# Optimization experiments

Hardware: AMD Instinct MI355X
Metric: run time of the kernel (lower is better)

The kernel has to match this reference:

```python
import jax, jax.numpy as jnp
import numpy as np

N, E, G = 100000, 1600000, 512
F_IN, H = 226, 128
BN_EPS = 1e-5

def _params(key):
    ks = jax.random.split(key, 34)
    p = {}
    dims = [(F_IN, H), (H, H), (H, H), (H, H)]
    i = 0
    for l, (din, dout) in enumerate(dims, start=1):
        p[f"W{l}a"] = jax.random.normal(ks[i], (din, dout), jnp.float32) * 0.05; i += 1
        p[f"b{l}a"] = jnp.zeros((dout,), jnp.float32)
        p[f"g{l}"] = jnp.ones((dout,), jnp.float32)
        p[f"be{l}"] = jnp.zeros((dout,), jnp.float32)
        p[f"rm{l}"] = jax.random.normal(ks[i], (dout,), jnp.float32) * 0.01; i += 1
        p[f"rv{l}"] = jnp.ones((dout,), jnp.float32)
        p[f"W{l}b"] = jax.random.normal(ks[i], (dout, dout), jnp.float32) * 0.05; i += 1
        p[f"b{l}b"] = jnp.zeros((dout,), jnp.float32)
    p["Wl"] = jax.random.normal(ks[i], (H, 1), jnp.float32) * 0.05
    p["bl"] = jnp.zeros((1,), jnp.float32)
    return p

def setup_inputs() -> dict:
    key = jax.random.key(0)
    k1, k2, k3, kp = jax.random.split(key, 4)
    inp = {
        "x": jax.random.normal(k1, (N, F_IN), jnp.float32),
        "edge_index": jax.random.randint(k2, (2, E), 0, N, jnp.int64),
        "batch": jnp.sort(jax.random.randint(k3, (N,), 0, G, jnp.int64)),
    }
    inp.update(_params(kp))
    return inp

def _gin_layer(x, src, dst, Wa, ba, g, be, rm, rv, Wb, bb):
    # GINConv (eps=0): mlp(x + sum_{j in N(i)} x_j)
    agg = jax.ops.segment_sum(x[src], dst, num_segments=N)  # [N,H] scatter-add
    h = (x + agg) @ Wa + ba
    h = g * (h - rm) * jax.lax.rsqrt(rv + BN_EPS) + be  # eval-mode BatchNorm1d
    h = jax.nn.relu(h)
    h = h @ Wb + bb
    return jax.nn.relu(h)  # outer F.relu after conv

def reference(x, edge_index, batch,
              W1a, b1a, g1, be1, rm1, rv1, W1b, b1b,
              W2a, b2a, g2, be2, rm2, rv2, W2b, b2b,
              W3a, b3a, g3, be3, rm3, rv3, W3b, b3b,
              W4a, b4a, g4, be4, rm4, rv4, W4b, b4b,
              Wl, bl):
    src, dst = edge_index[0], edge_index[1]
    h = _gin_layer(x, src, dst, W1a, b1a, g1, be1, rm1, rv1, W1b, b1b)
    h = _gin_layer(h, src, dst, W2a, b2a, g2, be2, rm2, rv2, W2b, b2b)
    h = _gin_layer(h, src, dst, W3a, b3a, g3, be3, rm3, rv3, W3b, b3b)
    h = _gin_layer(h, src, dst, W4a, b4a, g4, be4, rm4, rv4, W4b, b4b)
    # global mean pool over graphs
    sums = jax.ops.segment_sum(h, batch, num_segments=G)          # [G,H]
    cnts = jax.ops.segment_sum(jnp.ones((N,), h.dtype), batch, num_segments=G)
    pooled = sums / jnp.maximum(cnts, 1.0)[:, None]
    return pooled @ Wl + bl  # [G,1]
```

## Files before the change

kernel.cpp:

```cpp
#include <hip/hip_runtime.h>

#define NN 100000
#define NE 1600000
#define NG 512
#define FIN 226
#define HD 128
#define BN_EPS 1e-5f
#define NBUK 196
#define BCAP 10016

typedef __attribute__((ext_vector_type(8))) __bf16 bf16x8;
typedef __attribute__((ext_vector_type(8))) short short8;
typedef __attribute__((ext_vector_type(8))) unsigned short ushort8;
typedef __attribute__((ext_vector_type(4))) float f32x4;
typedef __attribute__((ext_vector_type(2))) float f32x2;

#define BC(x) __builtin_bit_cast(bf16x8, x)

__device__ inline unsigned short f2bf(float v) {
  unsigned u = __builtin_bit_cast(unsigned, v);
  return (unsigned short)((u + 0x7FFFu + ((u >> 16) & 1u)) >> 16);
}
__device__ inline float bf2f(unsigned short b) {
  return __builtin_bit_cast(float, (unsigned)b << 16);
}

__global__ __launch_bounds__(256) void k_bucket(const int* __restrict__ src,
                                                const int* __restrict__ dst,
                                                int* __restrict__ gcur,
                                                unsigned* __restrict__ pairs) {
  __shared__ int sd[4096];
  __shared__ int ss[4096];
  __shared__ int sh[NBUK];
  __shared__ int sexcl[NBUK];
  __shared__ int scur[NBUK];
  __shared__ int sbase[NBUK];
  __shared__ int wsum[4];
  const int tid = threadIdx.x;
  const int i0 = blockIdx.x * 4096;
  #pragma unroll
  for (int j = 0; j < 16; ++j) {
    int e = i0 + j * 256 + tid;
    sd[j * 256 + tid] = (e < NE) ? __builtin_nontemporal_load(dst + e) : -1;
    ss[j * 256 + tid] = (e < NE) ? __builtin_nontemporal_load(src + e) : 0;
  }
  if (tid < NBUK) sh[tid] = 0;
  __syncthreads();
  #pragma unroll
  for (int j = 0; j < 16; ++j) {
    int d = sd[j * 256 + tid];
    if (d >= 0) atomicAdd(&sh[d >> 9], 1);
  }
  __syncthreads();
  {
    int v = (tid < NBUK) ? sh[tid] : 0;
    int lane = tid & 63, w = tid >> 6;
    int incl = v;
    #pragma unroll
    for (int o = 1; o < 64; o <<= 1) {
      int u = __shfl_up(incl, o);
      if (lane >= o) incl += u;
    }
    if (lane == 63) wsum[w] = incl;
    __syncthreads();
    int off = 0;
    for (int k = 0; k < w; ++k) off += wsum[k];
    if (tid < NBUK) {
      int ex = off + incl - v;
      sexcl[tid] = ex;
      scur[tid] = ex;
      sbase[tid] = (v > 0) ? atomicAdd(&gcur[tid], v) : 0;
    }
  }
  __syncthreads();
  #pragma unroll
  for (int j = 0; j < 16; ++j) {
    int d = sd[j * 256 + tid];
    if (d >= 0) {
      int b = d >> 9;
      int lp = atomicAdd(&scur[b], 1);
      unsigned pk = ((unsigned)(d & 511) << 17) | (unsigned)ss[j * 256 + tid];
      pairs[(size_t)b * BCAP + sbase[b] + (lp - sexcl[b])] = pk;
    }
  }
}

__global__ __launch_bounds__(256) void k_bscan(const int* __restrict__ gcur,
                                               int* __restrict__ bucket_base,
                                               int* __restrict__ row_ptr) {
  __shared__ int wsum[4];
  const int tid = threadIdx.x;
  int v = (tid < NBUK) ? gcur[tid] : 0;
  int lane = tid & 63, w = tid >> 6;
  int incl = v;
  #pragma unroll
  for (int o = 1; o < 64; o <<= 1) {
    int u = __shfl_up(incl, o);
    if (lane >= o) incl += u;
  }
  if (lane == 63) wsum[w] = incl;
  __syncthreads();
  int off = 0;
  for (int k = 0; k < w; ++k) off += wsum[k];
  if (tid < NBUK) bucket_base[tid] = off + incl - v;
  if (tid == 0) row_ptr[NN] = NE;
}

__global__ __launch_bounds__(256) void k_pass2(const unsigned* __restrict__ pairs,
                                               const int* __restrict__ gcur,
                                               const int* __restrict__ bucket_base,
                                               int* __restrict__ row_ptr,
                                               int* __restrict__ col_idx) {
  __shared__ unsigned spk[BCAP];
  __shared__ int h[512];
  __shared__ int cur[512];
  __shared__ int wsum[4];
  const int b = blockIdx.x;
  const int tid = threadIdx.x;
  const int cnt = gcur[b];
  const int base = bucket_base[b];
  for (int i = tid; i < cnt; i += 256) spk[i] = pairs[(size_t)b * BCAP + i];
  h[tid] = 0; h[tid + 256] = 0;
  __syncthreads();
  for (int i = tid; i < cnt; i += 256) atomicAdd(&h[spk[i] >> 17], 1);
  __syncthreads();
  int c0 = h[2 * tid], c1 = h[2 * tid + 1];
  {
    int v = c0 + c1;
    int lane = tid & 63, w = tid >> 6;
    int incl = v;
    #pragma unroll
    for (int o = 1; o < 64; o <<= 1) {
      int u = __shfl_up(incl, o);
      if (lane >= o) incl += u;
    }
    if (lane == 63) wsum[w] = incl;
    __syncthreads();
    int off = 0;
    for (int k = 0; k < w; ++k) off += wsum[k];
    int e0 = off + incl - v;
    int e1 = e0 + c0;
    int node0 = b * 512 + 2 * tid;
    if (node0 < NN) row_ptr[node0] = base + e0;
    if (node0 + 1 < NN) row_ptr[node0 + 1] = base + e1;
    cur[2 * tid] = e0;
    cur[2 * tid + 1] = e1;
  }
  __syncthreads();
  for (int i = tid; i < cnt; i += 256) {
    unsigned pk = spk[i];
    int dl = pk >> 17;
    int p = atomicAdd(&cur[dl], 1);
    col_idx[base + p] = (int)(pk & 0x1FFFFu);
  }
}

struct PrepArgs {
  const float* W[9];
  const float* g[9];
  const float* rv[9];
  unsigned short* out[9];
  int k0[9];
  int K[9];
  const float* ba[4];
  const float* gg[4];
  const float* be[4];
  const float* rm[4];
  const float* rvv[4];
  float* bout;
};

__global__ __launch_bounds__(256) void k_prep(PrepArgs a) {
  int id = blockIdx.x * 256 + threadIdx.x;
  if (id < 9 * 16384) {
    int chunk = id >> 14;
    int r = id & 16383;
    int kk = r >> 7;
    int n = r & 127;
    float s = a.g[chunk] ? a.g[chunk][n] * rsqrtf(a.rv[chunk][n] + BN_EPS) : 1.f;
    int kg = a.k0[chunk] + kk;
    float v = (kg < a.K[chunk]) ? a.W[chunk][(size_t)kg * HD + n] * s : 0.f;
    unsigned short hb = f2bf(v);
    unsigned short lb = f2bf(v - bf2f(hb));
    int idx = n * 128 + (kk ^ ((n & 7) << 3));
    a.out[chunk][idx] = hb;
    a.out[chunk][16384 + idx] = lb;
  } else {
    int t = id - 9 * 16384;
    if (t < 512) {
      int l = t >> 7, c = t & 127;
      float s = a.gg[l][c] * rsqrtf(a.rvv[l][c] + BN_EPS);
      a.bout[l * 128 + c] = a.ba[l][c] * s + a.be[l][c] - a.rm[l][c] * s;
    }
  }
}

__global__ __launch_bounds__(256) void k_mgemm1(const float* __restrict__ A,
                                                const unsigned short* __restrict__ Wz,
                                                unsigned short* __restrict__ out,
                                                int K, int nchunks) {
  __shared__ unsigned short sW[32768];
  const int tid = threadIdx.x;
  const int wv = tid >> 6, ln = tid & 63;
  const int l15 = ln & 15, l4 = ln >> 4;
  const int m0 = blockIdx.x * 128 + wv * 32;
  f32x4 acc[2][8] = {};
  const int sw = (l15 & 7) << 3;
  int kofs[4];
  #pragma unroll
  for (int ks = 0; ks < 4; ++ks) kofs[ks] = (((ks * 32 + l4 * 8) ^ sw)) + l15 * 128;

  for (int c = 0; c < nchunks; ++c) {
    {
      const ushort8* src = (const ushort8*)(Wz + (size_t)c * 32768);
      ushort8* dst = (ushort8*)sW;
      #pragma unroll
      for (int i = 0; i < 16; ++i) dst[tid + i * 256] = src[tid + i * 256];
    }
    __syncthreads();
    const int kc = c * 128;
    #pragma unroll
    for (int ks = 0; ks < 4; ++ks) {
      const int kbase = kc + ks * 32 + l4 * 8;
      const bool tail = (kc + ks * 32 + 32) > K;
      short8 ah[2], al[2];
      #pragma unroll
      for (int mf = 0; mf < 2; ++mf) {
        const int row = m0 + mf * 16 + l15;
        float v[8];
        if (row < NN && !tail) {
          const f32x2* ap = (const f32x2*)(A + (size_t)row * K + kbase);
          #pragma unroll
          for (int q = 0; q < 4; ++q) {
            f32x2 t = __builtin_nontemporal_load(ap + q);
            v[2 * q] = t[0]; v[2 * q + 1] = t[1];
          }
        } else if (row < NN) {
          #pragma unroll
          for (int j = 0; j < 8; ++j) {
            int k = kbase + j;
            v[j] = (k < K) ? A[(size_t)row * K + k] : 0.f;
          }
        } else {
          #pragma unroll
          for (int j = 0; j < 8; ++j) v[j] = 0.f;
        }
        #pragma unroll
        for (int j = 0; j < 8; ++j) {
          unsigned short hb = f2bf(v[j]);
          ah[mf][j] = (short)hb;
          al[mf][j] = (short)f2bf(v[j] - bf2f(hb));
        }
      }
      #pragma unroll
      for (int n = 0; n < 8; ++n) {
        const int idx = n * 2048 + kofs[ks];
        short8 bh = *(const short8*)&sW[idx];
        short8 bl = *(const short8*)&sW[idx + 16384];
        #pragma unroll
        for (int mf = 0; mf < 2; ++mf) {
          acc[mf][n] = __builtin_amdgcn_mfma_f32_16x16x32_bf16(BC(ah[mf]), BC(bh), acc[mf][n], 0, 0, 0);
          acc[mf][n] = __builtin_amdgcn_mfma_f32_16x16x32_bf16(BC(ah[mf]), BC(bl), acc[mf][n], 0, 0, 0);
          acc[mf][n] = __builtin_amdgcn_mfma_f32_16x16x32_bf16(BC(al[mf]), BC(bh), acc[mf][n], 0, 0, 0);
        }
      }
    }
    __syncthreads();
  }
  #pragma unroll
  for (int mf = 0; mf < 2; ++mf) {
    #pragma unroll
    for (int n = 0; n < 8; ++n) {
      const int col = n * 16 + l15;
      #pragma unroll
      for (int r = 0; r < 4; ++r) {
        const int row = m0 + mf * 16 + l4 * 4 + r;
        if (row < NN) out[(size_t)row * HD + col] = f2bf(acc[mf][n][r]);
      }
    }
  }
}

template <int BIAS, int RELU>
__global__ __launch_bounds__(256) void k_mgemmB(const unsigned short* __restrict__ A,
                                                const unsigned short* __restrict__ Wz,
                                                const float* __restrict__ bias,
                                                unsigned short* __restrict__ out) {
  __shared__ unsigned short sW[32768];
  const int tid = threadIdx.x;
  const int wv = tid >> 6, ln = tid & 63;
  const int l15 = ln & 15, l4 = ln >> 4;
  const int m0 = blockIdx.x * 128 + wv * 32;
  f32x4 acc[2][8] = {};
  const int sw = (l15 & 7) << 3;
  {
    const ushort8* src = (const ushort8*)Wz;
    ushort8* dst = (ushort8*)sW;
    #pragma unroll
    for (int i = 0; i < 16; ++i) dst[tid + i * 256] = src[tid + i * 256];
  }
  __syncthreads();
  #pragma unroll
  for (int ks = 0; ks < 4; ++ks) {
    const int kbase = ks * 32 + l4 * 8;
    short8 a[2];
    #pragma unroll
    for (int mf = 0; mf < 2; ++mf) {
      const int row = m0 + mf * 16 + l15;
      if (row < NN) a[mf] = *(const short8*)(A + (size_t)row * HD + kbase);
      else a[mf] = short8{0, 0, 0, 0, 0, 0, 0, 0};
    }
    const int kof = (kbase ^ sw) + l15 * 128;
    #pragma unroll
    for (int n = 0; n < 8; ++n) {
      const int idx = n * 2048 + kof;
      short8 bh = *(const short8*)&sW[idx];
      short8 bl = *(const short8*)&sW[idx + 16384];
      #pragma unroll
      for (int mf = 0; mf < 2; ++mf) {
        acc[mf][n] = __builtin_amdgcn_mfma_f32_16x16x32_bf16(BC(a[mf]), BC(bh), acc[mf][n], 0, 0, 0);
        acc[mf][n] = __builtin_amdgcn_mfma_f32_16x16x32_bf16(BC(a[mf]), BC(bl), acc[mf][n], 0, 0, 0);
      }
    }
  }
  #pragma unroll
  for (int mf = 0; mf < 2; ++mf) {
    #pragma unroll
    for (int n = 0; n < 8; ++n) {
      const int col = n * 16 + l15;
      float bv = BIAS ? bias[col] : 0.f;
      #pragma unroll
      for (int r = 0; r < 4; ++r) {
        const int row = m0 + mf * 16 + l4 * 4 + r;
        if (row < NN) {
          float o = acc[mf][n][r] + bv;
          if (RELU) o = fmaxf(o, 0.f);
          out[(size_t)row * HD + col] = f2bf(o);
        }
      }
    }
  }
}

__global__ __launch_bounds__(256) void k_fused(const unsigned short* __restrict__ H,
                                               const unsigned short* __restrict__ Wzb,
                                               const float* __restrict__ bb,
                                               const unsigned short* __restrict__ Wza,
                                               unsigned short* __restrict__ Yout) {
  __shared__ unsigned short sB[16384];
  __shared__ unsigned short sA2[16384];
  __shared__ unsigned short sX[8192];
  const int tid = threadIdx.x;
  const int wv = tid >> 6, ln = tid & 63;
  const int l15 = ln & 15, l4 = ln >> 4;
  const int m0 = blockIdx.x * 128 + wv * 32;
  const int sw = (l15 & 7) << 3;
  f32x4 acc2[2][8] = {};

  short8 a[2][4];
  #pragma unroll
  for (int mf = 0; mf < 2; ++mf) {
    const int row = m0 + mf * 16 + l15;
    #pragma unroll
    for (int ks = 0; ks < 4; ++ks) {
      if (row < NN) a[mf][ks] = *(const short8*)(H + (size_t)row * HD + ks * 32 + l4 * 8);
      else a[mf][ks] = short8{0, 0, 0, 0, 0, 0, 0, 0};
    }
  }

  #pragma unroll 1
  for (int p = 0; p < 2; ++p) {
    {
      ushort8* d = (ushort8*)sB;
      const ushort8* s1 = (const ushort8*)(Wzb + p * 8192);
      const ushort8* s2 = (const ushort8*)(Wzb + 16384 + p * 8192);
      #pragma unroll
      for (int i = 0; i < 4; ++i) d[tid + i * 256] = s1[tid + i * 256];
      #pragma unroll
      for (int i = 0; i < 4; ++i) d[1024 + tid + i * 256] = s2[tid + i * 256];
    }
    {
      ushort8* d2 = (ushort8*)sA2;
      const ushort8* sa = (const ushort8*)Wza;
      #pragma unroll
      for (int i = 0; i < 4; ++i) {
        int idx = tid + i * 256;
        int n = idx >> 3, q8 = idx & 7;
        d2[idx] = sa[n * 16 + p * 8 + q8];
      }
      #pragma unroll
      for (int i = 0; i < 4; ++i) {
        int idx = tid + i * 256;
        int n = idx >> 3, q8 = idx & 7;
        d2[1024 + idx] = sa[2048 + n * 16 + p * 8 + q8];
      }
    }
    __syncthreads();

    f32x4 acc1[2][4] = {};
    #pragma unroll
    for (int ks = 0; ks < 4; ++ks) {
      const int kof = (ks * 32 + l4 * 8) ^ sw;
      #pragma unroll
      for (int nf = 0; nf < 4; ++nf) {
        const int idx = (nf * 16 + l15) * 128 + kof;
        short8 bh = *(const short8*)&sB[idx];
        short8 bl = *(const short8*)&sB[8192 + idx];
        #pragma unroll
        for (int mf = 0; mf < 2; ++mf) {
          acc1[mf][nf] = __builtin_amdgcn_mfma_f32_16x16x32_bf16(BC(a[mf][ks]), BC(bh), acc1[mf][nf], 0, 0, 0);
          acc1[mf][nf] = __builtin_amdgcn_mfma_f32_16x16x32_bf16(BC(a[mf][ks]), BC(bl), acc1[mf][nf], 0, 0, 0);
        }
      }
    }
    #pragma unroll
    for (int mf = 0; mf < 2; ++mf) {
      #pragma unroll
      for (int nf = 0; nf < 4; ++nf) {
        const int colL = nf * 16 + l15;
        const float bv = bb[p * 64 + colL];
        #pragma unroll
        for (int r = 0; r < 4; ++r) {
          const int rowL = wv * 32 + mf * 16 + l4 * 4 + r;
          sX[rowL * 64 + (colL ^ ((rowL & 7) << 3))] = f2bf(fmaxf(acc1[mf][nf][r] + bv, 0.f));
        }
      }
    }
    #pragma unroll
    for (int ks2 = 0; ks2 < 2; ++ks2) {
      const int xkof = (ks2 * 32 + l4 * 8) ^ sw;
      short8 xf[2];
      #pragma unroll
      for (int mf = 0; mf < 2; ++mf) {
        const int rowL = wv * 32 + mf * 16 + l15;
        xf[mf] = *(const short8*)&sX[rowL * 64 + xkof];
      }
      #pragma unroll
      for (int nf = 0; nf < 8; ++nf) {
        const int idx = (nf * 16 + l15) * 64 + xkof;
        short8 wh = *(const short8*)&sA2[idx];
        short8 wl = *(const short8*)&sA2[8192 + idx];
        #pragma unroll
        for (int mf = 0; mf < 2; ++mf) {
          acc2[mf][nf] = __builtin_amdgcn_mfma_f32_16x16x32_bf16(BC(xf[mf]), BC(wh), acc2[mf][nf], 0, 0, 0);
          acc2[mf][nf] = __builtin_amdgcn_mfma_f32_16x16x32_bf16(BC(xf[mf]), BC(wl), acc2[mf][nf], 0, 0, 0);
        }
      }
    }
    __syncthreads();
  }
  #pragma unroll
  for (int mf = 0; mf < 2; ++mf) {
    #pragma unroll
    for (int n = 0; n < 8; ++n) {
      const int col = n * 16 + l15;
      #pragma unroll
      for (int r = 0; r < 4; ++r) {
        const int row = m0 + mf * 16 + l4 * 4 + r;
        if (row < NN) Yout[(size_t)row * HD + col] = f2bf(acc2[mf][n][r]);
      }
    }
  }
}

__global__ __launch_bounds__(256) void k_agg(const unsigned short* __restrict__ y,
                                             const int* __restrict__ row_ptr,
                                             const int* __restrict__ col_idx,
                                             const float* __restrict__ bias,
                                             unsigned short* __restrict__ h) {
  const int node = blockIdx.x * 4 + (threadIdx.x >> 6);
  const int ln = threadIdx.x & 63;
  const int l15 = ln & 15, grp = ln >> 4;
  if (node >= NN) return;
  float acc[8] = {};
  const int beg = row_ptr[node], end = row_ptr[node + 1];
  int e = beg;
  for (; e + 16 <= end; e += 16) {
    const int s0 = __builtin_nontemporal_load(col_idx + e + grp);
    const int s1 = __builtin_nontemporal_load(col_idx + e + 4 + grp);
    const int s2 = __builtin_nontemporal_load(col_idx + e + 8 + grp);
    const int s3 = __builtin_nontemporal_load(col_idx + e + 12 + grp);
    const ushort8 v0 = *(const ushort8*)(y + (size_t)s0 * HD + l15 * 8);
    const ushort8 v1 = *(const ushort8*)(y + (size_t)s1 * HD + l15 * 8);
    const ushort8 v2 = *(const ushort8*)(y + (size_t)s2 * HD + l15 * 8);
    const ushort8 v3 = *(const ushort8*)(y + (size_t)s3 * HD + l15 * 8);
    #pragma unroll
    for (int j = 0; j < 8; ++j)
      acc[j] += (bf2f((unsigned short)v0[j]) + bf2f((unsigned short)v1[j])) +
                (bf2f((unsigned short)v2[j]) + bf2f((unsigned short)v3[j]));
  }
  for (; e + 8 <= end; e += 8) {
    const int s0 = __builtin_nontemporal_load(col_idx + e + grp);
    const int s1 = __builtin_nontemporal_load(col_idx + e + 4 + grp);
    const ushort8 v0 = *(const ushort8*)(y + (size_t)s0 * HD + l15 * 8);
    const ushort8 v1 = *(const ushort8*)(y + (size_t)s1 * HD + l15 * 8);
    #pragma unroll
    for (int j = 0; j < 8; ++j)
      acc[j] += bf2f((unsigned short)v0[j]) + bf2f((unsigned short)v1[j]);
  }
  if (e + 4 <= end) {
    const int s0 = __builtin_nontemporal_load(col_idx + e + grp);
    const ushort8 v0 = *(const ushort8*)(y + (size_t)s0 * HD + l15 * 8);
    #pragma unroll
    for (int j = 0; j < 8; ++j) acc[j] += bf2f((unsigned short)v0[j]);
    e += 4;
  }
  if (e + grp < end) {
    const int s0 = col_idx[e + grp];
    const ushort8 v0 = *(const ushort8*)(y + (size_t)s0 * HD + l15 * 8);
    #pragma unroll
    for (int j = 0; j < 8; ++j) acc[j] += bf2f((unsigned short)v0[j]);
  }
  #pragma unroll
  for (int j = 0; j < 8; ++j) {
    acc[j] += __shfl_xor(acc[j], 16);
    acc[j] += __shfl_xor(acc[j], 32);
  }
  const ushort8 sv = *(const ushort8*)(y + (size_t)node * HD + l15 * 8);
  const f32x4* b4 = (const f32x4*)(bias + l15 * 8);
  const f32x4 b0 = b4[0], b1 = b4[1];
  ushort8 o;
  #pragma unroll
  for (int j = 0; j < 8; ++j) {
    const float bj = (j < 4) ? b0[j] : b1[j - 4];
    o[j] = (unsigned short)f2bf(fmaxf(acc[j] + bf2f((unsigned short)sv[j]) + bj, 0.f));
  }
  if (grp == 0) *(ushort8*)(h + (size_t)node * HD + l15 * 8) = o;
}

__global__ __launch_bounds__(256) void k_pool2(const unsigned short* __restrict__ h,
                                               const int* __restrict__ batch,
                                               const float* __restrict__ Wl,
                                               float* __restrict__ sums,
                                               float* __restrict__ cnts) {
  __shared__ float sb[NG];
  __shared__ int sc[NG];
  const int tid = threadIdx.x;
  for (int i = tid; i < NG; i += 256) { sb[i] = 0.f; sc[i] = 0; }
  __syncthreads();
  const int wv = tid >> 6, ln = tid & 63;
  const float2 w2 = reinterpret_cast<const float2*>(Wl)[ln];
  #pragma unroll 1
  for (int i = 0; i < 16; ++i) {
    const int node = blockIdx.x * 64 + wv * 16 + i;
    if (node < NN) {
      const ushort2 hv = reinterpret_cast<const ushort2*>(h)[(size_t)node * 64 + ln];
      float d = bf2f(hv.x) * w2.x + bf2f(hv.y) * w2.y;
      #pragma unroll
      for (int off = 32; off > 0; off >>= 1) d += __shfl_down(d, off);
      if (ln == 0) {
        const int g = batch[node];
        atomicAdd(&sb[g], d);
        atomicAdd(&sc[g], 1);
      }
    }
  }
  __syncthreads();
  for (int i = tid; i < NG; i += 256)
    if (sc[i]) { atomicAdd(&sums[i], sb[i]); atomicAdd(&cnts[i], (float)sc[i]); }
}

__global__ void k_final(const float* __restrict__ sums, const float* __restrict__ cnts,
                        const float* __restrict__ bl, float* __restrict__ out) {
  int g = blockIdx.x * 256 + threadIdx.x;
  if (g < NG) out[g] = sums[g] / fmaxf(cnts[g], 1.f) + bl[0];
}

extern "C" void kernel_launch(void* const* d_in, const int* in_sizes, int n_in,
                              void* d_out, int out_size, void* d_ws, size_t ws_size,
                              hipStream_t stream) {
  const float* x = (const float*)d_in[0];
  const int* edges = (const int*)d_in[1];
  const int* batch = (const int*)d_in[2];
  const int* e_src = edges;
  const int* e_dst = edges + NE;
  const float* Wl = (const float*)d_in[35];
  const float* bl = (const float*)d_in[36];
  float* out = (float*)d_out;
  auto P = [&](int l, int which) -> const float* {
    return (const float*)d_in[3 + (l - 1) * 8 + which];
  };

  char* ws = (char*)d_ws;
  size_t off = 0;
  auto take = [&](size_t bytes) -> void* {
    void* p = ws + off;
    off = (off + bytes + 255) & ~(size_t)255;
    return p;
  };
  unsigned short* Y = (unsigned short*)take((size_t)NN * HD * 2);
  unsigned short* H = (unsigned short*)take((size_t)NN * HD * 2);
  unsigned short* X = (unsigned short*)take((size_t)NN * HD * 2);
  int* row_ptr = (int*)take((size_t)(NN + 1) * 4);
  int* col_idx = (int*)take((size_t)NE * 4);
  unsigned* pairs = (unsigned*)take((size_t)NBUK * BCAP * 4);
  int* gcur = (int*)take((size_t)NBUK * 4);
  int* bucket_base = (int*)take((size_t)NBUK * 4);
  unsigned short* Wza[4];
  unsigned short* Wzb[4];
  Wza[0] = (unsigned short*)take((size_t)2 * 32768 * 2);
  for (int l = 1; l < 4; ++l) Wza[l] = (unsigned short*)take((size_t)32768 * 2);
  for (int l = 0; l < 4; ++l) Wzb[l] = (unsigned short*)take((size_t)32768 * 2);
  float* bf = (float*)take((size_t)4 * HD * 4);
  float* psum = (float*)take((size_t)NG * 4 * 2);
  float* pcnt = psum + NG;

  hipMemsetAsync(gcur, 0, (size_t)NBUK * 4, stream);
  k_bucket<<<(NE + 4095) / 4096, 256, 0, stream>>>(e_src, e_dst, gcur, pairs);
  k_bscan<<<1, 256, 0, stream>>>(gcur, bucket_base, row_ptr);
  k_pass2<<<NBUK, 256, 0, stream>>>(pairs, gcur, bucket_base, row_ptr, col_idx);

  PrepArgs pa;
  for (int c = 0; c < 9; ++c) {
    if (c < 2) { pa.W[c] = P(1, 0); pa.g[c] = P(1, 2); pa.rv[c] = P(1, 5);
                 pa.out[c] = Wza[0] + c * 32768; pa.k0[c] = c * 128; pa.K[c] = FIN; }
    else if (c < 5) { int l = c - 1; pa.W[c] = P(l + 1, 0); pa.g[c] = P(l + 1, 2);
                      pa.rv[c] = P(l + 1, 5); pa.out[c] = Wza[l]; pa.k0[c] = 0; pa.K[c] = HD; }
    else { int l = c - 5; pa.W[c] = P(l + 1, 6); pa.g[c] = nullptr; pa.rv[c] = nullptr;
           pa.out[c] = Wzb[l]; pa.k0[c] = 0; pa.K[c] = HD; }
  }
  for (int l = 0; l < 4; ++l) {
    pa.ba[l] = P(l + 1, 1); pa.gg[l] = P(l + 1, 2); pa.be[l] = P(l + 1, 3);
    pa.rm[l] = P(l + 1, 4); pa.rvv[l] = P(l + 1, 5);
  }
  pa.bout = bf;
  k_prep<<<(9 * 16384 + 512 + 255) / 256, 256, 0, stream>>>(pa);

  hipMemsetAsync(psum, 0, (size_t)NG * 8, stream);

  const int gemm_grid = (NN + 127) / 128;
  k_mgemm1<<<gemm_grid, 256, 0, stream>>>(x, Wza[0], Y, FIN, 2);
  for (int l = 1; l <= 3; ++l) {
    k_agg<<<NN / 4, 256, 0, stream>>>(Y, row_ptr, col_idx, bf + (l - 1) * HD, H);
    k_fused<<<gemm_grid, 256, 0, stream>>>(H, Wzb[l - 1], P(l, 7), Wza[l], Y);
  }
  k_agg<<<NN / 4, 256, 0, stream>>>(Y, row_ptr, col_idx, bf + 3 * HD, H);
  k_mgemmB<1, 1><<<gemm_grid, 256, 0, stream>>>(H, Wzb[3], P(4, 7), X);
  k_pool2<<<(NN + 63) / 64, 256, 0, stream>>>(X, batch, Wl, psum, pcnt);
  k_final<<<(NG + 255) / 256, 256, 0, stream>>>(psum, pcnt, bl, out);
}
```

Measured before the change: 522.0 us.

## Drop split-bf16 weight low parts, fuse last GEMM into pooling, merge bucket scan

Weights are now stored as a single bf16 value instead of a hi/lo pair, which removes one MFMA per tile and halves the weight shared-memory loads and footprint. The final layer's second GEMM is fused with the mean-pool dot product, so the X intermediate is no longer written and read back. The bucket prefix scan is folded into k_pass2, which saves one kernel launch. The cost is lower numerical precision, since weight rounding error is no longer compensated.

```diff
diff --git a/kernel.cpp b/kernel.cpp
--- a/kernel.cpp
+++ b/kernel.cpp
@@ -85,40 +85,36 @@
   }
 }
 
-__global__ __launch_bounds__(256) void k_bscan(const int* __restrict__ gcur,
-                                               int* __restrict__ bucket_base,
-                                               int* __restrict__ row_ptr) {
-  __shared__ int wsum[4];
-  const int tid = threadIdx.x;
-  int v = (tid < NBUK) ? gcur[tid] : 0;
-  int lane = tid & 63, w = tid >> 6;
-  int incl = v;
-  #pragma unroll
-  for (int o = 1; o < 64; o <<= 1) {
-    int u = __shfl_up(incl, o);
-    if (lane >= o) incl += u;
-  }
-  if (lane == 63) wsum[w] = incl;
-  __syncthreads();
-  int off = 0;
-  for (int k = 0; k < w; ++k) off += wsum[k];
-  if (tid < NBUK) bucket_base[tid] = off + incl - v;
-  if (tid == 0) row_ptr[NN] = NE;
-}
-
 __global__ __launch_bounds__(256) void k_pass2(const unsigned* __restrict__ pairs,
                                                const int* __restrict__ gcur,
-                                               const int* __restrict__ bucket_base,
                                                int* __restrict__ row_ptr,
                                                int* __restrict__ col_idx) {
   __shared__ unsigned spk[BCAP];
   __shared__ int h[512];
   __shared__ int cur[512];
   __shared__ int wsum[4];
+  __shared__ int s_base;
   const int b = blockIdx.x;
   const int tid = threadIdx.x;
+  {
+    int v = (tid < NBUK) ? gcur[tid] : 0;
+    int lane = tid & 63, w = tid >> 6;
+    int incl = v;
+    #pragma unroll
+    for (int o = 1; o < 64; o <<= 1) {
+      int u = __shfl_up(incl, o);
+      if (lane >= o) incl += u;
+    }
+    if (lane == 63) wsum[w] = incl;
+    __syncthreads();
+    int off = 0;
+    for (int k = 0; k < w; ++k) off += wsum[k];
+    if (tid == b) s_base = off + incl - v;
+    if (b == 0 && tid == 0) row_ptr[NN] = NE;
+  }
   const int cnt = gcur[b];
-  const int base = bucket_base[b];
+  __syncthreads();
+  const int base = s_base;
   for (int i = tid; i < cnt; i += 256) spk[i] = pairs[(size_t)b * BCAP + i];
   h[tid] = 0; h[tid + 256] = 0;
   __syncthreads();
@@ -180,11 +176,8 @@
     float s = a.g[chunk] ? a.g[chunk][n] * rsqrtf(a.rv[chunk][n] + BN_EPS) : 1.f;
     int kg = a.k0[chunk] + kk;
     float v = (kg < a.K[chunk]) ? a.W[chunk][(size_t)kg * HD + n] * s : 0.f;
-    unsigned short hb = f2bf(v);
-    unsigned short lb = f2bf(v - bf2f(hb));
     int idx = n * 128 + (kk ^ ((n & 7) << 3));
-    a.out[chunk][idx] = hb;
-    a.out[chunk][16384 + idx] = lb;
+    a.out[chunk][idx] = f2bf(v);
   } else {
     int t = id - 9 * 16384;
     if (t < 512) {
@@ -199,7 +192,7 @@
                                                 const unsigned short* __restrict__ Wz,
                                                 unsigned short* __restrict__ out,
                                                 int K, int nchunks) {
-  __shared__ unsigned short sW[32768];
+  __shared__ unsigned short sW[16384];
   const int tid = threadIdx.x;
   const int wv = tid >> 6, ln = tid & 63;
   const int l15 = ln & 15, l4 = ln >> 4;
@@ -212,10 +205,10 @@
 
   for (int c = 0; c < nchunks; ++c) {
     {
-      const ushort8* src = (const ushort8*)(Wz + (size_t)c * 32768);
+      const ushort8* src = (const ushort8*)(Wz + (size_t)c * 16384);
       ushort8* dst = (ushort8*)sW;
       #pragma unroll
-      for (int i = 0; i < 16; ++i) dst[tid + i * 256] = src[tid + i * 256];
+      for (int i = 0; i < 8; ++i) dst[tid + i * 256] = src[tid + i * 256];
     }
     __syncthreads();
     const int kc = c * 128;
@@ -254,13 +247,10 @@
       }
       #pragma unroll
       for (int n = 0; n < 8; ++n) {
-        const int idx = n * 2048 + kofs[ks];
-        short8 bh = *(const short8*)&sW[idx];
-        short8 bl = *(const short8*)&sW[idx + 16384];
+        short8 bh = *(const short8*)&sW[n * 2048 + kofs[ks]];
         #pragma unroll
         for (int mf = 0; mf < 2; ++mf) {
           acc[mf][n] = __builtin_amdgcn_mfma_f32_16x16x32_bf16(BC(ah[mf]), BC(bh), acc[mf][n], 0, 0, 0);
-          acc[mf][n] = __builtin_amdgcn_mfma_f32_16x16x32_bf16(BC(ah[mf]), BC(bl), acc[mf][n], 0, 0, 0);
           acc[mf][n] = __builtin_amdgcn_mfma_f32_16x16x32_bf16(BC(al[mf]), BC(bh), acc[mf][n], 0, 0, 0);
         }
       }
@@ -276,67 +266,6 @@
       for (int r = 0; r < 4; ++r) {
         const int row = m0 + mf * 16 + l4 * 4 + r;
         if (row < NN) out[(size_t)row * HD + col] = f2bf(acc[mf][n][r]);
-      }
-    }
-  }
-}
-
-template <int BIAS, int RELU>
-__global__ __launch_bounds__(256) void k_mgemmB(const unsigned short* __restrict__ A,
-                                                const unsigned short* __restrict__ Wz,
-                                                const float* __restrict__ bias,
-                                                unsigned short* __restrict__ out) {
-  __shared__ unsigned short sW[32768];
-  const int tid = threadIdx.x;
-  const int wv = tid >> 6, ln = tid & 63;
-  const int l15 = ln & 15, l4 = ln >> 4;
-  const int m0 = blockIdx.x * 128 + wv * 32;
-  f32x4 acc[2][8] = {};
-  const int sw = (l15 & 7) << 3;
-  {
-    const ushort8* src = (const ushort8*)Wz;
-    ushort8* dst = (ushort8*)sW;
-    #pragma unroll
-    for (int i = 0; i < 16; ++i) dst[tid + i * 256] = src[tid + i * 256];
-  }
-  __syncthreads();
-  #pragma unroll
-  for (int ks = 0; ks < 4; ++ks) {
-    const int kbase = ks * 32 + l4 * 8;
-    short8 a[2];
-    #pragma unroll
-    for (int mf = 0; mf < 2; ++mf) {
-      const int row = m0 + mf * 16 + l15;
-      if (row < NN) a[mf] = *(const short8*)(A + (size_t)row * HD + kbase);
-      else a[mf] = short8{0, 0, 0, 0, 0, 0, 0, 0};
-    }
-    const int kof = (kbase ^ sw) + l15 * 128;
-    #pragma unroll
-    for (int n = 0; n < 8; ++n) {
-      const int idx = n * 2048 + kof;
-      short8 bh = *(const short8*)&sW[idx];
-      short8 bl = *(const short8*)&sW[idx + 16384];
-      #pragma unroll
-      for (int mf = 0; mf < 2; ++mf) {
-        acc[mf][n] = __builtin_amdgcn_mfma_f32_16x16x32_bf16(BC(a[mf]), BC(bh), acc[mf][n], 0, 0, 0);
-        acc[mf][n] = __builtin_amdgcn_mfma_f32_16x16x32_bf16(BC(a[mf]), BC(bl), acc[mf][n], 0, 0, 0);
-      }
-    }
-  }
-  #pragma unroll
-  for (int mf = 0; mf < 2; ++mf) {
-    #pragma unroll
-    for (int n = 0; n < 8; ++n) {
-      const int col = n * 16 + l15;
-      float bv = BIAS ? bias[col] : 0.f;
-      #pragma unroll
-      for (int r = 0; r < 4; ++r) {
-        const int row = m0 + mf * 16 + l4 * 4 + r;
-        if (row < NN) {
-          float o = acc[mf][n][r] + bv;
-          if (RELU) o = fmaxf(o, 0.f);
-          out[(size_t)row * HD + col] = f2bf(o);
-        }
       }
     }
   }
@@ -347,9 +276,10 @@
                                                const float* __restrict__ bb,
                                                const unsigned short* __restrict__ Wza,
                                                unsigned short* __restrict__ Yout) {
-  __shared__ unsigned short sB[16384];
-  __shared__ unsigned short sA2[16384];
-  __shared__ unsigned short sX[8192];
+  __shared__ __align__(16) char smem[49152];
+  unsigned short* sB = (unsigned short*)smem;
+  unsigned short* sA2 = (unsigned short*)(smem + 16384);
+  unsigned short* sX = (unsigned short*)(smem + 32768);
   const int tid = threadIdx.x;
   const int wv = tid >> 6, ln = tid & 63;
   const int l15 = ln & 15, l4 = ln >> 4;
@@ -373,11 +303,8 @@
     {
       ushort8* d = (ushort8*)sB;
       const ushort8* s1 = (const ushort8*)(Wzb + p * 8192);
-      const ushort8* s2 = (const ushort8*)(Wzb + 16384 + p * 8192);
       #pragma unroll
       for (int i = 0; i < 4; ++i) d[tid + i * 256] = s1[tid + i * 256];
-      #pragma unroll
-      for (int i = 0; i < 4; ++i) d[1024 + tid + i * 256] = s2[tid + i * 256];
     }
     {
       ushort8* d2 = (ushort8*)sA2;
@@ -388,12 +315,6 @@
         int n = idx >> 3, q8 = idx & 7;
         d2[idx] = sa[n * 16 + p * 8 + q8];
       }
-      #pragma unroll
-      for (int i = 0; i < 4; ++i) {
-        int idx = tid + i * 256;
-        int n = idx >> 3, q8 = idx & 7;
-        d2[1024 + idx] = sa[2048 + n * 16 + p * 8 + q8];
-      }
     }
     __syncthreads();
 
@@ -403,14 +324,10 @@
       const int kof = (ks * 32 + l4 * 8) ^ sw;
       #pragma unroll
       for (int nf = 0; nf < 4; ++nf) {
-        const int idx = (nf * 16 + l15) * 128 + kof;
-        short8 bh = *(const short8*)&sB[idx];
-        short8 bl = *(const short8*)&sB[8192 + idx];
+        short8 bh = *(const short8*)&sB[(nf * 16 + l15) * 128 + kof];
         #pragma unroll
-        for (int mf = 0; mf < 2; ++mf) {
+        for (int mf = 0; mf < 2; ++mf)
           acc1[mf][nf] = __builtin_amdgcn_mfma_f32_16x16x32_bf16(BC(a[mf][ks]), BC(bh), acc1[mf][nf], 0, 0, 0);
-          acc1[mf][nf] = __builtin_amdgcn_mfma_f32_16x16x32_bf16(BC(a[mf][ks]), BC(bl), acc1[mf][nf], 0, 0, 0);
-        }
       }
     }
     #pragma unroll
@@ -437,14 +354,10 @@
       }
       #pragma unroll
       for (int nf = 0; nf < 8; ++nf) {
-        const int idx = (nf * 16 + l15) * 64 + xkof;
-        short8 wh = *(const short8*)&sA2[idx];
-        short8 wl = *(const short8*)&sA2[8192 + idx];
+        short8 wh = *(const short8*)&sA2[(nf * 16 + l15) * 64 + xkof];
         #pragma unroll
-        for (int mf = 0; mf < 2; ++mf) {
+        for (int mf = 0; mf < 2; ++mf)
           acc2[mf][nf] = __builtin_amdgcn_mfma_f32_16x16x32_bf16(BC(xf[mf]), BC(wh), acc2[mf][nf], 0, 0, 0);
-          acc2[mf][nf] = __builtin_amdgcn_mfma_f32_16x16x32_bf16(BC(xf[mf]), BC(wl), acc2[mf][nf], 0, 0, 0);
-        }
       }
     }
     __syncthreads();
@@ -528,30 +441,78 @@
   if (grp == 0) *(ushort8*)(h + (size_t)node * HD + l15 * 8) = o;
 }
 
-__global__ __launch_bounds__(256) void k_pool2(const unsigned short* __restrict__ h,
+__global__ __launch_bounds__(256) void k_bpool(const unsigned short* __restrict__ H,
+                                               const unsigned short* __restrict__ Wzb,
+                                               const float* __restrict__ bb,
+                                               const float* __restrict__ Wl,
                                                const int* __restrict__ batch,
-                                               const float* __restrict__ Wl,
                                                float* __restrict__ sums,
                                                float* __restrict__ cnts) {
+  __shared__ unsigned short sW[16384];
   __shared__ float sb[NG];
   __shared__ int sc[NG];
   const int tid = threadIdx.x;
+  const int wv = tid >> 6, ln = tid & 63;
+  const int l15 = ln & 15, l4 = ln >> 4;
+  const int m0 = blockIdx.x * 128 + wv * 32;
+  const int sw = (l15 & 7) << 3;
   for (int i = tid; i < NG; i += 256) { sb[i] = 0.f; sc[i] = 0; }
-  __syncthreads();
-  const int wv = tid >> 6, ln = tid & 63;
-  const float2 w2 = reinterpret_cast<const float2*>(Wl)[ln];
-  #pragma unroll 1
-  for (int i = 0; i < 16; ++i) {
-    const int node = blockIdx.x * 64 + wv * 16 + i;
-    if (node < NN) {
-      const ushort2 hv = reinterpret_cast<const ushort2*>(h)[(size_t)node * 64 + ln];
-      float d = bf2f(hv.x) * w2.x + bf2f(hv.y) * w2.y;
-      #pragma unroll
-      for (int off = 32; off > 0; off >>= 1) d += __shfl_down(d, off);
-      if (ln == 0) {
-        const int g = batch[node];
-        atomicAdd(&sb[g], d);
-        atomicAdd(&sc[g], 1);
+  {
+    const ushort8* src = (const ushort8*)Wzb;
+    ushort8* dst = (ushort8*)sW;
+    #pragma unroll
+    for (int i = 0; i < 8; ++i) dst[tid + i * 256] = src[tid + i * 256];
+  }
+  __syncthreads();
+  f32x4 acc[2][8] = {};
+  #pragma unroll
+  for (int ks = 0; ks < 4; ++ks) {
+    const int kbase = ks * 32 + l4 * 8;
+    short8 a[2];
+    #pragma unroll
+    for (int mf = 0; mf < 2; ++mf) {
+      const int row = m0 + mf * 16 + l15;
+      if (row < NN) a[mf] = *(const short8*)(H + (size_t)row * HD + kbase);
+      else a[mf] = short8{0, 0, 0, 0, 0, 0, 0, 0};
+    }
+    const int kof = (kbase ^ sw) + l15 * 128;
+    #pragma unroll
+    for (int n = 0; n < 8; ++n) {
+      short8 bh = *(const short8*)&sW[n * 2048 + kof];
+      #pragma unroll
+      for (int mf = 0; mf < 2; ++mf)
+        acc[mf][n] = __builtin_amdgcn_mfma_f32_16x16x32_bf16(BC(a[mf]), BC(bh), acc[mf][n], 0, 0, 0);
+    }
+  }
+  float pdot[2][4] = {};
+  #pragma unroll
+  for (int mf = 0; mf < 2; ++mf) {
+    #pragma unroll
+    for (int n = 0; n < 8; ++n) {
+      const int col = n * 16 + l15;
+      const float bv = bb[col];
+      const float wl = Wl[col];
+      #pragma unroll
+      for (int r = 0; r < 4; ++r)
+        pdot[mf][r] += fmaxf(acc[mf][n][r] + bv, 0.f) * wl;
+    }
+  }
+  #pragma unroll
+  for (int mf = 0; mf < 2; ++mf) {
+    #pragma unroll
+    for (int r = 0; r < 4; ++r) {
+      float d = pdot[mf][r];
+      d += __shfl_xor(d, 1);
+      d += __shfl_xor(d, 2);
+      d += __shfl_xor(d, 4);
+      d += __shfl_xor(d, 8);
+      if (l15 == 0) {
+        const int row = m0 + mf * 16 + l4 * 4 + r;
+        if (row < NN) {
+          const int g = batch[row];
+          atomicAdd(&sb[g], d);
+          atomicAdd(&sc[g], 1);
+        }
       }
     }
   }
@@ -590,30 +551,27 @@
   };
   unsigned short* Y = (unsigned short*)take((size_t)NN * HD * 2);
   unsigned short* H = (unsigned short*)take((size_t)NN * HD * 2);
-  unsigned short* X = (unsigned short*)take((size_t)NN * HD * 2);
   int* row_ptr = (int*)take((size_t)(NN + 1) * 4);
   int* col_idx = (int*)take((size_t)NE * 4);
   unsigned* pairs = (unsigned*)take((size_t)NBUK * BCAP * 4);
   int* gcur = (int*)take((size_t)NBUK * 4);
-  int* bucket_base = (int*)take((size_t)NBUK * 4);
   unsigned short* Wza[4];
   unsigned short* Wzb[4];
-  Wza[0] = (unsigned short*)take((size_t)2 * 32768 * 2);
-  for (int l = 1; l < 4; ++l) Wza[l] = (unsigned short*)take((size_t)32768 * 2);
-  for (int l = 0; l < 4; ++l) Wzb[l] = (unsigned short*)take((size_t)32768 * 2);
+  Wza[0] = (unsigned short*)take((size_t)2 * 16384 * 2);
+  for (int l = 1; l < 4; ++l) Wza[l] = (unsigned short*)take((size_t)16384 * 2);
+  for (int l = 0; l < 4; ++l) Wzb[l] = (unsigned short*)take((size_t)16384 * 2);
   float* bf = (float*)take((size_t)4 * HD * 4);
   float* psum = (float*)take((size_t)NG * 4 * 2);
   float* pcnt = psum + NG;
 
   hipMemsetAsync(gcur, 0, (size_t)NBUK * 4, stream);
   k_bucket<<<(NE + 4095) / 4096, 256, 0, stream>>>(e_src, e_dst, gcur, pairs);
-  k_bscan<<<1, 256, 0, stream>>>(gcur, bucket_base, row_ptr);
-  k_pass2<<<NBUK, 256, 0, stream>>>(pairs, gcur, bucket_base, row_ptr, col_idx);
+  k_pass2<<<NBUK, 256, 0, stream>>>(pairs, gcur, row_ptr, col_idx);
 
   PrepArgs pa;
   for (int c = 0; c < 9; ++c) {
     if (c < 2) { pa.W[c] = P(1, 0); pa.g[c] = P(1, 2); pa.rv[c] = P(1, 5);
-                 pa.out[c] = Wza[0] + c * 32768; pa.k0[c] = c * 128; pa.K[c] = FIN; }
+                 pa.out[c] = Wza[0] + c * 16384; pa.k0[c] = c * 128; pa.K[c] = FIN; }
     else if (c < 5) { int l = c - 1; pa.W[c] = P(l + 1, 0); pa.g[c] = P(l + 1, 2);
                       pa.rv[c] = P(l + 1, 5); pa.out[c] = Wza[l]; pa.k0[c] = 0; pa.K[c] = HD; }
     else { int l = c - 5; pa.W[c] = P(l + 1, 6); pa.g[c] = nullptr; pa.rv[c] = nullptr;
@@ -628,14 +586,13 @@
 
   hipMemsetAsync(psum, 0, (size_t)NG * 8, stream);
 
-  const int gemm_grid = (NN + 127) / 128;
-  k_mgemm1<<<gemm_grid, 256, 0, stream>>>(x, Wza[0], Y, FIN, 2);
+  const int grid = (NN + 127) / 128;
+  k_mgemm1<<<grid, 256, 0, stream>>>(x, Wza[0], Y, FIN, 2);
   for (int l = 1; l <= 3; ++l) {
     k_agg<<<NN / 4, 256, 0, stream>>>(Y, row_ptr, col_idx, bf + (l - 1) * HD, H);
-    k_fused<<<gemm_grid, 256, 0, stream>>>(H, Wzb[l - 1], P(l, 7), Wza[l], Y);
+    k_fused<<<grid, 256, 0, stream>>>(H, Wzb[l - 1], P(l, 7), Wza[l], Y);
   }
   k_agg<<<NN / 4, 256, 0, stream>>>(Y, row_ptr, col_idx, bf + 3 * HD, H);
-  k_mgemmB<1, 1><<<gemm_grid, 256, 0, stream>>>(H, Wzb[3], P(4, 7), X);
-  k_pool2<<<(NN + 63) / 64, 256, 0, stream>>>(X, batch, Wl, psum, pcnt);
+  k_bpool<<<grid, 256, 0, stream>>>(H, Wzb[3], P(4, 7), Wl, batch, psum, pcnt);
   k_final<<<(NG + 255) / 256, 256, 0, stream>>>(psum, pcnt, bl, out);
 }
```

Measured after the change: 470.3 us. -9.9%, faster.
